# Performance work log

Hardware: AMD Instinct MI355X
Metric: run time of the kernel (lower is better)

## Reference

```python
import jax, jax.numpy as jnp
import numpy as np

H = 1024   # hidden_size
I = 64     # input_window_size
OUT = 12   # fc output (hardcoded in module)

def _uniform(key, shape):
    return jax.random.uniform(key, shape, jnp.float32, -0.1, 0.1)

def setup_inputs() -> dict:
    key = jax.random.key(0)
    ks = jax.random.split(key, 9)
    x = jax.random.normal(ks[0], (256, 512, I), jnp.float32)
    # gate order i, f, g, o stacked along first axis -> [4H, in_dim]
    Wx0 = _uniform(ks[1], (4 * H, I))
    Wh0 = _uniform(ks[2], (4 * H, H))
    b0  = _uniform(ks[3], (4 * H,))
    Wx1 = _uniform(ks[4], (4 * H, H))
    Wh1 = _uniform(ks[5], (4 * H, H))
    b1  = _uniform(ks[6], (4 * H,))
    fc_W = _uniform(ks[7], (OUT, H))
    fc_b = _uniform(ks[8], (OUT,))
    return {"x": x, "Wx0": Wx0, "Wh0": Wh0, "b0": b0,
            "Wx1": Wx1, "Wh1": Wh1, "b1": b1,
            "fc_W": fc_W, "fc_b": fc_b}

def _cell(x_t, h_prev, c_prev, Wx, Wh, b):
    # fused gate GEMM: same math as 8 separate per-gate matmuls
    gates = x_t @ Wx.T + h_prev @ Wh.T + b  # [B, 4H]
    i_t = jax.nn.sigmoid(gates[:, 0 * H:1 * H])
    f_t = jax.nn.sigmoid(gates[:, 1 * H:2 * H])
    g_t = jnp.tanh(gates[:, 2 * H:3 * H])
    o_t = jax.nn.sigmoid(gates[:, 3 * H:4 * H])
    c_t = f_t * c_prev + i_t * g_t
    h_t = o_t * jnp.tanh(c_t)
    return h_t, c_t

def reference(x, Wx0, Wh0, b0, Wx1, Wh1, b1, fc_W, fc_b):
    B = x.shape[0]
    h0 = jnp.zeros((B, H), x.dtype)
    init = (h0, h0, h0, h0)  # (h_l0, c_l0, h_l1, c_l1)

    def step(carry, x_t):
        h0_, c0_, h1_, c1_ = carry
        h0n, c0n = _cell(x_t, h0_, c0_, Wx0, Wh0, b0)
        h1n, c1n = _cell(h0n, h1_, c1_, Wx1, Wh1, b1)
        return (h0n, c0n, h1n, c1n), None

    xs = jnp.swapaxes(x, 0, 1)  # [T, B, I]
    (h0f, c0f, h1f, c1f), _ = jax.lax.scan(step, init, xs)
    return h1f @ fc_W.T + fc_b  # [B, 12]
```

## Files before the change

kernel.cpp:

```cpp
#include <hip/hip_runtime.h>


typedef unsigned int u32;
typedef unsigned short u16;
typedef __attribute__((ext_vector_type(8))) short bf16x8;
typedef __attribute__((ext_vector_type(4))) float f32x4;

#define MFMA __builtin_amdgcn_mfma_f32_16x16x32_bf16
#define HB (256 * 1024)

#define BARL() do {                                                            \
  asm volatile("s_waitcnt lgkmcnt(0)" ::: "memory");                           \
  __builtin_amdgcn_s_barrier();                                                \
  asm volatile("" ::: "memory");                                               \
} while (0)

__device__ __forceinline__ u16 f2bf(float f) {
  u32 u = __float_as_uint(f);
  u += 0x7fffu + ((u >> 16) & 1u);
  return (u16)(u >> 16);
}
__device__ __forceinline__ float sigm(float v) { return 1.f / (1.f + __expf(-v)); }
__device__ __forceinline__ float tanh_(float v) { return 1.f - 2.f / (__expf(2.f * v) + 1.f); }

__device__ __forceinline__ u32 ld_u32_sc01(const u32* p) {
  u32 v;
  asm volatile("global_load_dword %0, %1, off sc0 sc1\n\ts_waitcnt vmcnt(0)"
               : "=v"(v) : "v"(p) : "memory");
  return v;
}
__device__ __forceinline__ void st_u32_sc01(u32* p, u32 v) {
  asm volatile("global_store_dword %0, %1, off sc0 sc1" :: "v"(p), "v"(v) : "memory");
}
__device__ __forceinline__ void st_f32_sc01(float* p, float v) {
  asm volatile("global_store_dword %0, %1, off sc0 sc1" :: "v"(p), "v"(v) : "memory");
}

__global__ void __launch_bounds__(256) wconv(
    const float* __restrict__ Wx0, const float* __restrict__ Wh0,
    const float* __restrict__ Wx1, const float* __restrict__ Wh1,
    u16* __restrict__ W1p, u16* __restrict__ W0p, u16* __restrict__ X0p) {
  const u32 NG1 = 1048576u, NG0 = 524288u, NGX = 32768u;
  u32 g = blockIdx.x * 256u + threadIdx.x;
  const float* src; u16* dst;
  if (g < NG1) {
    u32 lane = g & 63u, f = (g >> 6) & 1u, jj = (g >> 7) & 1u, c = (g >> 8) & 7u;
    u32 kway = (g >> 11) & 3u, s = (g >> 13) & 1u, u0idx = g >> 14;
    u32 i15 = lane & 15u, kq = lane >> 4;
    u32 row = (2u * f + (i15 >> 3)) * 1024u + u0idx * 16u + s * 8u + (i15 & 7u);
    u32 k = (kway + 4u * (2u * c + jj)) * 32u + kq * 8u;
    src = (k < 1024u) ? Wx1 + (size_t)row * 1024 + k
                      : Wh1 + (size_t)row * 1024 + (k - 1024u);
    dst = W1p + (size_t)g * 8;
  } else if (g < NG1 + NG0) {
    u32 h = g - NG1;
    u32 lane = h & 63u, f = (h >> 6) & 1u, jj = (h >> 7) & 1u, c = (h >> 8) & 3u;
    u32 kway = (h >> 10) & 3u, s = (h >> 12) & 1u, u0idx = h >> 13;
    u32 i15 = lane & 15u, kq = lane >> 4;
    u32 row = (2u * f + (i15 >> 3)) * 1024u + u0idx * 16u + s * 8u + (i15 & 7u);
    u32 k = (kway + 4u * (2u * c + jj)) * 32u + kq * 8u;
    src = Wh0 + (size_t)row * 1024 + k;
    dst = W0p + (size_t)h * 8;
  } else if (g < NG1 + NG0 + NGX) {
    u32 h = g - NG1 - NG0;
    u32 lane = h & 63u, f = (h >> 6) & 1u, kway = (h >> 7) & 1u;
    u32 s = (h >> 8) & 1u, u0idx = h >> 9;
    u32 i15 = lane & 15u, kq = lane >> 4;
    u32 row = (2u * f + (i15 >> 3)) * 1024u + u0idx * 16u + s * 8u + (i15 & 7u);
    u32 k = kway * 32u + kq * 8u;
    src = Wx0 + (size_t)row * 64 + k;
    dst = X0p + (size_t)h * 8;
  } else return;
  float4 v0 = *(const float4*)src, v1 = *(const float4*)(src + 4);
  bf16x8 r;
  r[0] = (short)f2bf(v0.x); r[1] = (short)f2bf(v0.y);
  r[2] = (short)f2bf(v0.z); r[3] = (short)f2bf(v0.w);
  r[4] = (short)f2bf(v1.x); r[5] = (short)f2bf(v1.y);
  r[6] = (short)f2bf(v1.z); r[7] = (short)f2bf(v1.w);
  *(bf16x8*)dst = r;
}

#define LDW(bank, c) do {                                                      \
  u32 o0_ = bW[0] + (u32)((c) * 2048), o1_ = bW[1] + (u32)((c) * 2048);        \
  u32 o2_ = bW[2] + (u32)((c) * 2048), o3_ = bW[3] + (u32)((c) * 2048);        \
  asm volatile("" : "+v"(o0_), "+v"(o1_), "+v"(o2_), "+v"(o3_));               \
  _Pragma("unroll")                                                            \
  for (int jj_ = 0; jj_ < 2; ++jj_)                                            \
    _Pragma("unroll")                                                          \
    for (int f_ = 0; f_ < 2; ++f_) {                                           \
      W[bank][jj_][0][f_] = *(const bf16x8*)(WP + o0_ + (u32)(jj_*1024+f_*512));\
      W[bank][jj_][1][f_] = *(const bf16x8*)(WP + o1_ + (u32)(jj_*1024+f_*512));\
      W[bank][jj_][2][f_] = *(const bf16x8*)(WP + o2_ + (u32)(jj_*1024+f_*512));\
      W[bank][jj_][3][f_] = *(const bf16x8*)(WP + o3_ + (u32)(jj_*1024+f_*512));\
    }                                                                          \
} while (0)

#define CHUNK(bank) do {                                                       \
  _Pragma("unroll")                                                            \
  for (int jj_ = 0; jj_ < 2; ++jj_) {                                          \
    const int kin_ = (kway + (jj_ << 2)) << 5;                                 \
    _Pragma("unroll")                                                          \
    for (int mf_ = 0; mf_ < 4; ++mf_) {                                        \
      bf16x8 a_ = readA(mf_, kin_);                                            \
      _Pragma("unroll")                                                        \
      for (int s_ = 0; s_ < 4; ++s_)                                           \
        _Pragma("unroll")                                                      \
        for (int f_ = 0; f_ < 2; ++f_)                                         \
          acc[mf_][s_][f_] = MFMA(a_, W[bank][jj_][s_][f_],                    \
                                  acc[mf_][s_][f_], 0, 0, 0);                  \
    }                                                                          \
  }                                                                            \
} while (0)

__global__ void __launch_bounds__(256, 1)
lstm_persist(const float* __restrict__ x,
             const float* __restrict__ b0, const float* __restrict__ b1,
             const float* __restrict__ fcW, const float* __restrict__ fcb,
             const u16* __restrict__ W1p, const u16* __restrict__ W0p,
             const u16* __restrict__ X0p,
             u16* __restrict__ h0b, u16* __restrict__ h1b,
             float* __restrict__ h1f, u32* __restrict__ bar,
             float* __restrict__ out)
{
  const int tid = threadIdx.x, blk = blockIdx.x;
  const int lane = tid & 63, w = tid >> 6;
  const int kway = w;
  const int L = blk >> 7;
  const int sub = blk & 127;
  const int m0 = (sub >> 5) << 6;
  const int uidx = sub & 31;
  const int u0 = uidx << 5;

  __shared__ short Abuf[64 * 256];
  __shared__ float gA[64][132];
  __shared__ float gB[64][132];
  __shared__ float cbuf[64][32];

  for (int i = tid; i < 64 * 32; i += 256) ((float*)cbuf)[i] = 0.f;

  const int i15 = lane & 15, kq = lane >> 4;

  u32 bW[4], bX[4];
#pragma unroll
  for (int s_ = 0; s_ < 4; ++s_) {
    u32 key = (u32)((uidx << 2) + s_);
    bW[s_] = ((key << 2) | (u32)kway) * (L ? 16384u : 8192u) + (u32)lane * 8u;
    bX[s_] = ((key << 1) | (u32)kway) * 1024u + (u32)lane * 8u;
  }
  const u16* WP = L ? W1p : W0p;

  float bias[4][2];
#pragma unroll
  for (int s_ = 0; s_ < 4; ++s_)
#pragma unroll
    for (int f_ = 0; f_ < 2; ++f_) {
      int rowf = ((f_ << 1) + (i15 >> 3)) * 1024 + u0 + s_ * 8 + (i15 & 7);
      bias[s_][f_] = (kway == 0) ? (L ? b1[rowf] : b0[rowf]) : 0.f;
    }

  int grow[8], ldsoff[8];
#pragma unroll
  for (int cc = 0; cc < 8; ++cc) {
    int slot = cc * 256 + tid;
    int row = slot >> 5, c = slot & 31;
    grow[cc]   = ((m0 + row) << 10) + (c << 3);
    ldsoff[cc] = (row << 8) + ((c ^ (row & 7)) << 3);
  }

  bf16x8 v[8];
  auto stage_ld = [&](const u16* src, int kbase) {
#pragma unroll
    for (int cc = 0; cc < 8; ++cc)
      v[cc] = __builtin_nontemporal_load((const bf16x8*)(src + grow[cc] + kbase));
  };
  auto stage_st = [&]() {
#pragma unroll
    for (int cc = 0; cc < 8; ++cc)
      *(bf16x8*)&Abuf[ldsoff[cc]] = v[cc];
  };

  auto stage_x = [&](int t) {
    int row = tid >> 2, c4 = tid & 3;
    const float* g = x + ((size_t)(m0 + row) * 512 + t) * 64 + (c4 << 4);
    float4 a0 = *(const float4*)g,       a1 = *(const float4*)(g + 4);
    float4 a2 = *(const float4*)(g + 8), a3 = *(const float4*)(g + 12);
    bf16x8 r0, r1;
    r0[0] = (short)f2bf(a0.x); r0[1] = (short)f2bf(a0.y);
    r0[2] = (short)f2bf(a0.z); r0[3] = (short)f2bf(a0.w);
    r0[4] = (short)f2bf(a1.x); r0[5] = (short)f2bf(a1.y);
    r0[6] = (short)f2bf(a1.z); r0[7] = (short)f2bf(a1.w);
    r1[0] = (short)f2bf(a2.x); r1[1] = (short)f2bf(a2.y);
    r1[2] = (short)f2bf(a2.z); r1[3] = (short)f2bf(a2.w);
    r1[4] = (short)f2bf(a3.x); r1[5] = (short)f2bf(a3.y);
    r1[6] = (short)f2bf(a3.z); r1[7] = (short)f2bf(a3.w);
    int c = c4 << 1;
    *(bf16x8*)&Abuf[(row << 8) + (((c    ) ^ (row & 7)) << 3)] = r0;
    *(bf16x8*)&Abuf[(row << 8) + (((c + 1) ^ (row & 7)) << 3)] = r1;
  };

  auto readA = [&](int mf, int kin) -> bf16x8 {
    int row = (mf << 4) | i15;
    int c = ((kin >> 3) + kq) ^ (row & 7);
    return *(const bf16x8*)&Abuf[(row << 8) + (c << 3)];
  };

  bf16x8 W[2][2][4][2];
  f32x4 acc[4][4][2];

  auto acc_init = [&]() {
#pragma unroll
    for (int mf = 0; mf < 4; ++mf)
#pragma unroll
      for (int s_ = 0; s_ < 4; ++s_)
#pragma unroll
        for (int f_ = 0; f_ < 2; ++f_) {
          float bv = bias[s_][f_];
          acc[mf][s_][f_][0] = bv; acc[mf][s_][f_][1] = bv;
          acc[mf][s_][f_][2] = bv; acc[mf][s_][f_][3] = bv;
        }
  };

  auto reduce2 = [&]() {
    if (kway < 2) {
      float (*g)[132] = kway ? gB : gA;
#pragma unroll
      for (int mf = 0; mf < 4; ++mf)
#pragma unroll
        for (int s_ = 0; s_ < 4; ++s_)
#pragma unroll
          for (int f_ = 0; f_ < 2; ++f_)
#pragma unroll
            for (int r = 0; r < 4; ++r)
              g[(mf << 4) + (kq << 2) + r][(s_ << 5) + (f_ << 4) + i15] = acc[mf][s_][f_][r];
    }
    __syncthreads();
    if (kway >= 2) {
      float (*g)[132] = (kway == 3) ? gB : gA;
#pragma unroll
      for (int mf = 0; mf < 4; ++mf)
#pragma unroll
        for (int s_ = 0; s_ < 4; ++s_)
#pragma unroll
          for (int f_ = 0; f_ < 2; ++f_)
#pragma unroll
            for (int r = 0; r < 4; ++r)
              g[(mf << 4) + (kq << 2) + r][(s_ << 5) + (f_ << 4) + i15] += acc[mf][s_][f_][r];
    }
    __syncthreads();
  };

  auto ew = [&](u16* hdst, bool wf32) {
    int row = tid >> 2, un = (tid & 3) << 3;
    float hq[8];
#pragma unroll
    for (int q = 0; q < 8; ++q) {
      int u = un + q;
      int cb = ((u >> 3) << 5) | (u & 7);
      float gi = gA[row][cb]      + gB[row][cb];
      float gf = gA[row][cb + 8]  + gB[row][cb + 8];
      float gg = gA[row][cb + 16] + gB[row][cb + 16];
      float go = gA[row][cb + 24] + gB[row][cb + 24];
      float ii = sigm(gi), ff = sigm(gf), g2 = tanh_(gg), oo = sigm(go);
      float c = ff * cbuf[row][u] + ii * g2;
      cbuf[row][u] = c;
      hq[q] = oo * tanh_(c);
    }
    size_t idx = ((size_t)(m0 + row) << 10) + u0 + un;
#pragma unroll
    for (int q = 0; q < 4; ++q)
      st_u32_sc01((u32*)(hdst + idx + 2 * q),
                  (u32)f2bf(hq[2 * q]) | ((u32)f2bf(hq[2 * q + 1]) << 16));
    if (wf32) {
#pragma unroll
      for (int q = 0; q < 8; ++q) st_f32_sc01(h1f + idx + q, hq[q]);
    }
  };

  auto gridbar = [&](int t) {
    __syncthreads();
    if (tid == 0) {
      const int g = blk & 7;
      u32* gc   = bar + g * 32;
      u32* root = bar + 256;
      u32* gen  = bar + 288 + g * 32;
      const u32 p1 = (u32)(t + 1);
      __hip_atomic_fetch_add(gc, 1u, __ATOMIC_RELAXED, __HIP_MEMORY_SCOPE_AGENT);
      if (blk < 8) {
        while (ld_u32_sc01(gc) < 32u * p1) __builtin_amdgcn_s_sleep(4);
        __hip_atomic_fetch_add(root, 1u, __ATOMIC_RELAXED, __HIP_MEMORY_SCOPE_AGENT);
        while (ld_u32_sc01(root) < 8u * p1) __builtin_amdgcn_s_sleep(2);
        st_u32_sc01(gen, p1);
      } else {
        while (ld_u32_sc01(gen) < p1) __builtin_amdgcn_s_sleep(4);
      }
    }
    __syncthreads();
  };

  if (L == 0) {
#pragma unroll 1
    for (int t = 0; t <= 512; ++t) {
      if (t < 512) {
        const u16* h0rd = h0b + ((t + 1) & 1) * HB;
        u16* h0wr = h0b + (t & 1) * HB;
        acc_init();
        stage_x(t);
        stage_ld(h0rd, 0);
        bf16x8 X[4][2];
        if (kway < 2) {
          u32 ox0 = bX[0], ox1 = bX[1], ox2 = bX[2], ox3 = bX[3];
          asm volatile("" : "+v"(ox0), "+v"(ox1), "+v"(ox2), "+v"(ox3));
          X[0][0] = *(const bf16x8*)(X0p + ox0);
          X[0][1] = *(const bf16x8*)(X0p + ox0 + 512u);
          X[1][0] = *(const bf16x8*)(X0p + ox1);
          X[1][1] = *(const bf16x8*)(X0p + ox1 + 512u);
          X[2][0] = *(const bf16x8*)(X0p + ox2);
          X[2][1] = *(const bf16x8*)(X0p + ox2 + 512u);
          X[3][0] = *(const bf16x8*)(X0p + ox3);
          X[3][1] = *(const bf16x8*)(X0p + ox3 + 512u);
        }
        LDW(0, 0);
        BARL();
        if (kway < 2) {
          const int kin = kway << 5;
#pragma unroll
          for (int mf = 0; mf < 4; ++mf) {
            bf16x8 a = readA(mf, kin);
#pragma unroll
            for (int s_ = 0; s_ < 4; ++s_)
#pragma unroll
              for (int f_ = 0; f_ < 2; ++f_)
                acc[mf][s_][f_] = MFMA(a, X[s_][f_], acc[mf][s_][f_], 0, 0, 0);
          }
        }
        BARL();
        stage_st(); BARL();
        stage_ld(h0rd, 256); LDW(1, 1); CHUNK(0); BARL();
        stage_st(); BARL();
        stage_ld(h0rd, 512); LDW(0, 2); CHUNK(1); BARL();
        stage_st(); BARL();
        stage_ld(h0rd, 768); LDW(1, 3); CHUNK(0); BARL();
        stage_st(); BARL();
        CHUNK(1);
        reduce2();
        ew(h0wr, false);
      }
      gridbar(t);
    }
  } else {
#pragma unroll 1
    for (int t = 0; t <= 512; ++t) {
      if (t >= 1) {
        const u16* h0rd = h0b + ((t + 1) & 1) * HB;
        const u16* h1rd = h1b + (t & 1) * HB;
        u16* h1wr = h1b + ((t + 1) & 1) * HB;
        acc_init();
        stage_ld(h0rd, 0); LDW(0, 0);
        stage_st(); BARL();
        stage_ld(h0rd, 256); LDW(1, 1); CHUNK(0); BARL();
        stage_st(); BARL();
        stage_ld(h0rd, 512); LDW(0, 2); CHUNK(1); BARL();
        stage_st(); BARL();
        stage_ld(h0rd, 768); LDW(1, 3); CHUNK(0); BARL();
        stage_st(); BARL();
        stage_ld(h1rd, 0);   LDW(0, 4); CHUNK(1); BARL();
        stage_st(); BARL();
        stage_ld(h1rd, 256); LDW(1, 5); CHUNK(0); BARL();
        stage_st(); BARL();
        stage_ld(h1rd, 512); LDW(0, 6); CHUNK(1); BARL();
        stage_st(); BARL();
        stage_ld(h1rd, 768); LDW(1, 7); CHUNK(0); BARL();
        stage_st(); BARL();
        CHUNK(1);
        reduce2();
        ew(h1wr, t == 512);
      }
      gridbar(t);
    }
  }

  if (blk < 64) {
    const int row = (blk << 2) | w;
    const float* hrow = h1f + ((size_t)row << 10);
#pragma unroll 1
    for (int o = 0; o < 12; ++o) {
      const float* wrow = fcW + o * 1024;
      float p = 0.f;
#pragma unroll
      for (int j = 0; j < 16; ++j) {
        int k = (j << 6) | lane;
        p += __builtin_nontemporal_load(hrow + k) * wrow[k];
      }
#pragma unroll
      for (int off = 32; off > 0; off >>= 1) p += __shfl_down(p, off, 64);
      if (lane == 0) out[row * 12 + o] = p + fcb[o];
    }
  }
}

extern "C" void kernel_launch(void* const* d_in, const int* in_sizes, int n_in,
                              void* d_out, int out_size, void* d_ws, size_t ws_size,
                              hipStream_t stream) {
  (void)in_sizes; (void)n_in; (void)out_size; (void)ws_size;
  const float* x   = (const float*)d_in[0];
  const float* Wx0 = (const float*)d_in[1];
  const float* Wh0 = (const float*)d_in[2];
  const float* b0  = (const float*)d_in[3];
  const float* Wx1 = (const float*)d_in[4];
  const float* Wh1 = (const float*)d_in[5];
  const float* b1  = (const float*)d_in[6];
  const float* fcW = (const float*)d_in[7];
  const float* fcb = (const float*)d_in[8];

  char* ws = (char*)d_ws;
  u16* W1p   = (u16*)ws;
  u16* W0p   = (u16*)(ws + (16u << 20));
  u16* X0p   = (u16*)(ws + (24u << 20));
  u16* h0b   = (u16*)(ws + (25u << 20));
  u16* h1b   = (u16*)(ws + (26u << 20));
  float* h1f = (float*)(ws + (27u << 20));
  u32* bar   = (u32*)(ws + (28u << 20));

  hipMemsetAsync(ws + (25u << 20) + (1 << 19), 0, 1 << 19, stream);
  hipMemsetAsync(ws + (26u << 20) + (1 << 19), 0, 1 << 19, stream);
  hipMemsetAsync(bar, 0, 4096, stream);

  wconv<<<6272, 256, 0, stream>>>(Wx0, Wh0, Wx1, Wh1, W1p, W0p, X0p);
  lstm_persist<<<256, 256, 0, stream>>>(x, b0, b1, fcW, fcb,
                                        W1p, W0p, X0p,
                                        h0b, h1b, h1f, bar, (float*)d_out);
}
```

Measured before the change: 8.570 ms.

## Triple-buffer hidden-state register staging to prefetch three chunks ahead

Replaces the single register staging buffer for h-state chunks with three rotating register buffers. Global loads for up to three chunks are issued at the start of each timestep, before the x staging and weight loads. This is meant to hide global-memory latency on the recurrent critical path. It costs extra VGPRs (24 more bf16x8 registers) and adds a barrier after the last CHUNK, which could raise register pressure or cause spills in a kernel already launched with one block per CU.

```diff
diff --git a/kernel.cpp b/kernel.cpp
--- a/kernel.cpp
+++ b/kernel.cpp
@@ -95,6 +95,19 @@
     }                                                                          \
 } while (0)
 
+#define STAGE_LD(bk, src, kbase) do {                                          \
+  _Pragma("unroll")                                                            \
+  for (int cc = 0; cc < 8; ++cc)                                               \
+    v##bk[cc] = __builtin_nontemporal_load(                                    \
+        (const bf16x8*)((src) + grow[cc] + (kbase)));                          \
+} while (0)
+
+#define STAGE_ST(bk) do {                                                      \
+  _Pragma("unroll")                                                            \
+  for (int cc = 0; cc < 8; ++cc)                                               \
+    *(bf16x8*)&Abuf[ldsoff[cc]] = v##bk[cc];                                   \
+} while (0)
+
 #define CHUNK(bank) do {                                                       \
   _Pragma("unroll")                                                            \
   for (int jj_ = 0; jj_ < 2; ++jj_) {                                          \
@@ -167,17 +180,7 @@
     ldsoff[cc] = (row << 8) + ((c ^ (row & 7)) << 3);
   }
 
-  bf16x8 v[8];
-  auto stage_ld = [&](const u16* src, int kbase) {
-#pragma unroll
-    for (int cc = 0; cc < 8; ++cc)
-      v[cc] = __builtin_nontemporal_load((const bf16x8*)(src + grow[cc] + kbase));
-  };
-  auto stage_st = [&]() {
-#pragma unroll
-    for (int cc = 0; cc < 8; ++cc)
-      *(bf16x8*)&Abuf[ldsoff[cc]] = v[cc];
-  };
+  bf16x8 v0[8], v1[8], v2[8];
 
   auto stage_x = [&](int t) {
     int row = tid >> 2, c4 = tid & 3;
@@ -304,8 +307,11 @@
         const u16* h0rd = h0b + ((t + 1) & 1) * HB;
         u16* h0wr = h0b + (t & 1) * HB;
         acc_init();
+        STAGE_LD(0, h0rd, 0);
+        STAGE_LD(1, h0rd, 256);
+        STAGE_LD(2, h0rd, 512);
+        LDW(0, 0);
         stage_x(t);
-        stage_ld(h0rd, 0);
         bf16x8 X[4][2];
         if (kway < 2) {
           u32 ox0 = bX[0], ox1 = bX[1], ox2 = bX[2], ox3 = bX[3];
@@ -319,7 +325,6 @@
           X[3][0] = *(const bf16x8*)(X0p + ox3);
           X[3][1] = *(const bf16x8*)(X0p + ox3 + 512u);
         }
-        LDW(0, 0);
         BARL();
         if (kway < 2) {
           const int kin = kway << 5;
@@ -334,14 +339,10 @@
           }
         }
         BARL();
-        stage_st(); BARL();
-        stage_ld(h0rd, 256); LDW(1, 1); CHUNK(0); BARL();
-        stage_st(); BARL();
-        stage_ld(h0rd, 512); LDW(0, 2); CHUNK(1); BARL();
-        stage_st(); BARL();
-        stage_ld(h0rd, 768); LDW(1, 3); CHUNK(0); BARL();
-        stage_st(); BARL();
-        CHUNK(1);
+        STAGE_ST(0); BARL(); STAGE_LD(0, h0rd, 768); LDW(1, 1); CHUNK(0); BARL();
+        STAGE_ST(1); BARL(); LDW(0, 2); CHUNK(1); BARL();
+        STAGE_ST(2); BARL(); LDW(1, 3); CHUNK(0); BARL();
+        STAGE_ST(0); BARL(); CHUNK(1); BARL();
         reduce2();
         ew(h0wr, false);
       }
@@ -355,23 +356,18 @@
         const u16* h1rd = h1b + (t & 1) * HB;
         u16* h1wr = h1b + ((t + 1) & 1) * HB;
         acc_init();
-        stage_ld(h0rd, 0); LDW(0, 0);
-        stage_st(); BARL();
-        stage_ld(h0rd, 256); LDW(1, 1); CHUNK(0); BARL();
-        stage_st(); BARL();
-        stage_ld(h0rd, 512); LDW(0, 2); CHUNK(1); BARL();
-        stage_st(); BARL();
-        stage_ld(h0rd, 768); LDW(1, 3); CHUNK(0); BARL();
-        stage_st(); BARL();
-        stage_ld(h1rd, 0);   LDW(0, 4); CHUNK(1); BARL();
-        stage_st(); BARL();
-        stage_ld(h1rd, 256); LDW(1, 5); CHUNK(0); BARL();
-        stage_st(); BARL();
-        stage_ld(h1rd, 512); LDW(0, 6); CHUNK(1); BARL();
-        stage_st(); BARL();
-        stage_ld(h1rd, 768); LDW(1, 7); CHUNK(0); BARL();
-        stage_st(); BARL();
-        CHUNK(1);
+        STAGE_LD(0, h0rd, 0);
+        STAGE_LD(1, h0rd, 256);
+        STAGE_LD(2, h0rd, 512);
+        LDW(0, 0);
+        STAGE_ST(0); BARL(); STAGE_LD(0, h0rd, 768); LDW(1, 1); CHUNK(0); BARL();
+        STAGE_ST(1); BARL(); STAGE_LD(1, h1rd, 0);   LDW(0, 2); CHUNK(1); BARL();
+        STAGE_ST(2); BARL(); STAGE_LD(2, h1rd, 256); LDW(1, 3); CHUNK(0); BARL();
+        STAGE_ST(0); BARL(); STAGE_LD(0, h1rd, 512); LDW(0, 4); CHUNK(1); BARL();
+        STAGE_ST(1); BARL(); STAGE_LD(1, h1rd, 768); LDW(1, 5); CHUNK(0); BARL();
+        STAGE_ST(2); BARL(); LDW(0, 6); CHUNK(1); BARL();
+        STAGE_ST(0); BARL(); LDW(1, 7); CHUNK(0); BARL();
+        STAGE_ST(1); BARL(); CHUNK(1); BARL();
         reduce2();
         ew(h1wr, t == 512);
       }
```

New measurement: 8.593 ms. Within noise of the previous version (+0.3%).
